# Optimization experiments

Measured on AMD Instinct MI355X. Metric: run time of the kernel, lower is better.

The kernel has to match this reference:

```python
import jax, jax.numpy as jnp
import numpy as np

B, C_IN, C_INTER, H, W_DIM = 8, 512, 256, 64, 64


def setup_inputs() -> dict:
    key = jax.random.key(0)
    k1, k2, k3, k4 = jax.random.split(key, 4)
    x = jax.random.normal(k1, (B, C_IN, H, W_DIM), dtype=jnp.float32)
    pem_feats = jax.random.normal(k2, (B, C_INTER, H * W_DIM), dtype=jnp.float32)
    # 1x1 conv weight stored as [out, in] (kernel spatial dims are 1x1)
    W = jax.random.normal(k3, (C_INTER, C_IN), dtype=jnp.float32) * (1.0 / np.sqrt(C_IN))
    bias = jax.random.normal(k4, (C_INTER,), dtype=jnp.float32) * 0.01
    return {"x": x, "pem_feats": pem_feats, "W": W, "bias": bias}


def reference(x, pem_feats, W, bias):
    b, c, h, w = x.shape
    # 1x1 conv == channel-mixing GEMM: [b, inter, h, w]
    proj = jnp.einsum('bchw,oc->bohw', x, W) + bias[None, :, None, None]
    proj = proj.reshape(b, -1, h * w)                      # [b, inter, hw]
    # weights[b,i,j] = <proj[:, i], pem[:, j]>  -> [b, hw, hw], softmax over j
    scores = jnp.einsum('bci,bcj->bij', proj, pem_feats)
    weights = jax.nn.softmax(scores, axis=-1)
    # out[b,k,i] = sum_j weights[b,j,i] * pem[b,k,j]
    eam = jnp.einsum('bji,bkj->bki', weights, pem_feats)   # [b, inter, hw]
    return eam.reshape(b, -1, h, w)
```

## Files before the change

kernel.cpp:

```cpp
#include <hip/hip_runtime.h>
#include <math.h>

#define BATCH 8
#define CIN 512
#define CO 256
#define HW 4096
#define KT 32
#define NCHUNK 128
#define NSEG 4
#define SEGC (NCHUNK / NSEG)

typedef unsigned short ushort_t;
typedef unsigned int uint_t;
typedef __bf16 v8bf __attribute__((ext_vector_type(8)));
typedef _Float16 v8h __attribute__((ext_vector_type(8)));
typedef _Float16 v4h __attribute__((ext_vector_type(4)));
typedef float v4f __attribute__((ext_vector_type(4)));
typedef ushort_t u16x8 __attribute__((ext_vector_type(8)));

__device__ __forceinline__ ushort_t f2bf(float f) {
  uint_t u = __float_as_uint(f);
  u += 0x7FFFu + ((u >> 16) & 1u);
  return (ushort_t)(u >> 16);
}
__device__ __forceinline__ float bf2f(ushort_t h) {
  return __uint_as_float(((uint_t)h) << 16);
}
__device__ __forceinline__ ushort_t f2h(float f) {
  return __builtin_bit_cast(ushort_t, (_Float16)f);
}
__device__ __forceinline__ v4f mfma16(v8bf a, v8bf b, v4f c) {
  return __builtin_amdgcn_mfma_f32_16x16x32_bf16(a, b, c, 0, 0, 0);
}
__device__ __forceinline__ v4f mfma16h(v8h a, v8h b, v4f c) {
  return __builtin_amdgcn_mfma_f32_16x16x32_f16(a, b, c, 0, 0, 0);
}
__device__ __forceinline__ v8h lds_frag_h512(const unsigned char* base, int row, int cb) {
  uint4 v = *(const uint4*)(base + row * 512 + (((cb) ^ (row & 7)) << 4));
  return __builtin_bit_cast(v8h, v);
}
__device__ __forceinline__ v8bf lds_frag128(const unsigned char* base, int row, int cb) {
  uint4 v = *(const uint4*)(base + row * 128 + (((cb) ^ (row & 7)) << 4));
  return __builtin_bit_cast(v8bf, v);
}
__device__ __forceinline__ v8h lds_frag_h16(const unsigned char* base, int row, int cb) {
  uint4 v = *(const uint4*)(base + row * 256 + (((cb) ^ (row & 15)) << 4));
  return __builtin_bit_cast(v8h, v);
}
__device__ __forceinline__ void gll16(const void* g, void* l) {
  __builtin_amdgcn_global_load_lds(
      (const __attribute__((address_space(1))) unsigned int*)g,
      (__attribute__((address_space(3))) unsigned int*)l, 16, 0, 0);
}

__global__ __launch_bounds__(256) void k_w_split(
    const float* __restrict__ W, ushort_t* __restrict__ w_hi,
    ushort_t* __restrict__ w_lo) {
  int idx = blockIdx.x * 256 + threadIdx.x;
  size_t off = (size_t)idx * 8;
  float4 v0 = *(const float4*)&W[off];
  float4 v1 = *(const float4*)&W[off + 4];
  float f[8] = {v0.x, v0.y, v0.z, v0.w, v1.x, v1.y, v1.z, v1.w};
  u16x8 h, l;
#pragma unroll
  for (int j = 0; j < 8; ++j) {
    ushort_t hh = f2bf(f[j]);
    h[j] = hh;
    l[j] = f2bf(f[j] - bf2f(hh));
  }
  *(u16x8*)&w_hi[off] = h;
  *(u16x8*)&w_lo[off] = l;
}

__global__ __launch_bounds__(256) void k_tr_x(
    const float* __restrict__ x,
    ushort_t* __restrict__ xt_hi, ushort_t* __restrict__ xt_lo) {
  __shared__ float T[64][65];
  const int i0 = blockIdx.x * 64;
  const int c0 = blockIdx.y * 64;
  const int b  = blockIdx.z;
  const int t  = threadIdx.x;
  const int cl = t >> 4;
  const int i4 = (t & 15) * 4;
#pragma unroll
  for (int r = 0; r < 4; ++r) {
    int c = c0 + r * 16 + cl;
    size_t off = ((size_t)b * CIN + c) * HW + i0 + i4;
    float4 v = *(const float4*)&x[off];
    T[r * 16 + cl][i4 + 0] = v.x;
    T[r * 16 + cl][i4 + 1] = v.y;
    T[r * 16 + cl][i4 + 2] = v.z;
    T[r * 16 + cl][i4 + 3] = v.w;
  }
  __syncthreads();
  {
    int il = t >> 2;
    int cs = (t & 3) * 16;
    u16x8 h0, h1, l0, l1;
#pragma unroll
    for (int j = 0; j < 8; ++j) {
      float f = T[cs + j][il];
      ushort_t h = f2bf(f);
      h0[j] = h;
      l0[j] = f2bf(f - bf2f(h));
    }
#pragma unroll
    for (int j = 0; j < 8; ++j) {
      float f = T[cs + 8 + j][il];
      ushort_t h = f2bf(f);
      h1[j] = h;
      l1[j] = f2bf(f - bf2f(h));
    }
    size_t ro = ((size_t)b * HW + i0 + il) * CIN + c0 + cs;
    *(u16x8*)&xt_hi[ro]     = h0;
    *(u16x8*)&xt_hi[ro + 8] = h1;
    *(u16x8*)&xt_lo[ro]     = l0;
    *(u16x8*)&xt_lo[ro + 8] = l1;
  }
}

__global__ __launch_bounds__(256, 2) void k_proj_mfma(
    const ushort_t* __restrict__ xt_hi, const ushort_t* __restrict__ xt_lo,
    const ushort_t* __restrict__ w_hi, const ushort_t* __restrict__ w_lo,
    const float* __restrict__ bias, ushort_t* __restrict__ proj_h) {
  __shared__ __align__(16) unsigned char L[4][128 * 128];
  const int bid = blockIdx.x;
  const int b = bid & 7;
  const int rest = bid >> 3;
  const int xt = rest & 31;
  const int oh = rest >> 5;
  const int x0 = xt * 128;
  const int t = threadIdx.x;
  const int lane = t & 63, wave = t >> 6;

  v4f acc[2][8];
#pragma unroll
  for (int xf = 0; xf < 2; ++xf)
#pragma unroll
    for (int of = 0; of < 8; ++of) acc[xf][of] = (v4f){0.f, 0.f, 0.f, 0.f};

  float bias_of[8];
#pragma unroll
  for (int of = 0; of < 8; ++of)
    bias_of[of] = bias[oh * 128 + of * 16 + (lane & 15)];

  for (int ch = 0; ch < 8; ++ch) {
    const int c0 = ch * 64;
#pragma unroll
    for (int i = 0; i < 4; ++i) {
      int G = i * 256 + t;
      int r = G >> 3, sl = G & 7;
      int cg = (sl ^ (r & 7)) << 3;
      size_t xsrc = ((size_t)b * HW + x0 + r) * CIN + c0 + cg;
      size_t wsrc = ((size_t)(oh * 128 + r)) * CIN + c0 + cg;
      unsigned lb = (unsigned)((i * 256 + wave * 64) << 4);
      gll16(&xt_hi[xsrc], &L[0][lb]);
      gll16(&xt_lo[xsrc], &L[1][lb]);
      gll16(&w_hi[wsrc],  &L[2][lb]);
      gll16(&w_lo[wsrc],  &L[3][lb]);
    }
    __syncthreads();
#pragma unroll
    for (int st = 0; st < 2; ++st) {
      int cb = st * 4 + (lane >> 4);
      v8bf ah0 = lds_frag128(L[0], wave * 32 + (lane & 15), cb);
      v8bf ah1 = lds_frag128(L[0], wave * 32 + 16 + (lane & 15), cb);
      v8bf al0 = lds_frag128(L[1], wave * 32 + (lane & 15), cb);
      v8bf al1 = lds_frag128(L[1], wave * 32 + 16 + (lane & 15), cb);
#pragma unroll
      for (int of = 0; of < 8; ++of) {
        v8bf bh = lds_frag128(L[2], of * 16 + (lane & 15), cb);
        v8bf bl = lds_frag128(L[3], of * 16 + (lane & 15), cb);
        acc[0][of] = mfma16(ah0, bh, acc[0][of]);
        acc[0][of] = mfma16(ah0, bl, acc[0][of]);
        acc[0][of] = mfma16(al0, bh, acc[0][of]);
        acc[1][of] = mfma16(ah1, bh, acc[1][of]);
        acc[1][of] = mfma16(ah1, bl, acc[1][of]);
        acc[1][of] = mfma16(al1, bh, acc[1][of]);
      }
    }
    __syncthreads();
  }

  ushort_t* Th = (ushort_t*)&L[0][0];
#pragma unroll
  for (int xf = 0; xf < 2; ++xf)
#pragma unroll
    for (int of = 0; of < 8; ++of)
#pragma unroll
      for (int r = 0; r < 4; ++r) {
        int x_loc = wave * 32 + xf * 16 + (lane >> 4) * 4 + r;
        int o_loc = of * 16 + (lane & 15);
        Th[x_loc * 128 + o_loc] = f2h(acc[xf][of][r] + bias_of[of]);
      }
  __syncthreads();
  {
    int row = t >> 1, half = t & 1;
    size_t off = ((size_t)b * HW + x0 + row) * CO + oh * 128 + half * 64;
#pragma unroll
    for (int j = 0; j < 8; ++j)
      *(uint4*)&proj_h[off + j * 8] =
          *(const uint4*)&Th[row * 128 + half * 64 + j * 8];
  }
}

__global__ __launch_bounds__(256) void k_tr_pem(
    const float* __restrict__ pem,
    ushort_t* __restrict__ pem_t_h, ushort_t* __restrict__ pem_h) {
  __shared__ float T[64][65];
  const int y0 = blockIdx.x * 64;
  const int c0 = blockIdx.y * 64;
  const int b  = blockIdx.z;
  const int t  = threadIdx.x;
  const int cl = t >> 4;
  const int y4 = (t & 15) * 4;
#pragma unroll
  for (int r = 0; r < 4; ++r) {
    int c = c0 + r * 16 + cl;
    size_t off = ((size_t)b * CO + c) * HW + y0 + y4;
    float4 v = *(const float4*)&pem[off];
    ushort4 h;
    h.x = f2h(v.x); h.y = f2h(v.y); h.z = f2h(v.z); h.w = f2h(v.w);
    *(ushort4*)&pem_h[off] = h;
    T[r * 16 + cl][y4 + 0] = v.x;
    T[r * 16 + cl][y4 + 1] = v.y;
    T[r * 16 + cl][y4 + 2] = v.z;
    T[r * 16 + cl][y4 + 3] = v.w;
  }
  __syncthreads();
  {
    int yl = t >> 2;
    int cs = (t & 3) * 16;
    u16x8 h0, h1;
#pragma unroll
    for (int j = 0; j < 8; ++j) h0[j] = f2h(T[cs + j][yl]);
#pragma unroll
    for (int j = 0; j < 8; ++j) h1[j] = f2h(T[cs + 8 + j][yl]);
    size_t ro = ((size_t)b * HW + y0 + yl) * CO + c0 + cs;
    *(u16x8*)&pem_t_h[ro]     = h0;
    *(u16x8*)&pem_t_h[ro + 8] = h1;
  }
}

__global__ __launch_bounds__(256, 3) void k_pass1(
    const ushort_t* __restrict__ proj_h, const ushort_t* __restrict__ pem_t_h,
    _Float16* __restrict__ Ep, float* __restrict__ m_snap,
    float* __restrict__ m_seg, float* __restrict__ d_seg,
    int nb, int b_base) {
  __shared__ __align__(16) unsigned char pbuf[2][32 * 512];
  __shared__ __align__(16) unsigned char Etr[2][32 * 256];
  const int id = blockIdx.x;
  const int brel = id % nb;
  const int b = b_base + brel;
  const int rest = id / nb;
  const int xt = rest & 31;
  const int seg = rest >> 5;
  const int x0 = xt * 128;
  const int t = threadIdx.x;
  const int lane = t & 63, wave = t >> 6;
  const int xw = x0 + wave * 32;

  v8h Ah[2][8];
#pragma unroll
  for (int xf = 0; xf < 2; ++xf) {
    const size_t ro =
        ((size_t)b * HW + xw + xf * 16 + (lane & 15)) * CO + (lane >> 4) * 8;
#pragma unroll
    for (int st = 0; st < 8; ++st)
      Ah[xf][st] = __builtin_bit_cast(v8h, *(const uint4*)&proj_h[ro + st * 32]);
  }

  float m[2][4], d[2][4];
#pragma unroll
  for (int xf = 0; xf < 2; ++xf)
#pragma unroll
    for (int r = 0; r < 4; ++r) { m[xf][r] = -3.0e38f; d[xf][r] = 0.f; }

  auto stage = [&](int bufi, int tt) {
    const int yy0 = tt * 32;
#pragma unroll
    for (int i = 0; i < 4; ++i) {
      int G = i * 256 + t;
      int r = G >> 5, sl = G & 31;
      size_t so = ((size_t)b * HW + yy0 + r) * CO + ((sl ^ (r & 7)) << 3);
      unsigned lb = (unsigned)((i * 256 + wave * 64) << 4);
      gll16(&pem_t_h[so], &pbuf[bufi][lb]);
    }
  };

  const int tt0 = seg * SEGC;
  stage(0, tt0);
  __syncthreads();

  for (int tc = 0; tc < SEGC; ++tc) {
    const int tt = tt0 + tc;
    if (tc + 1 < SEGC) stage((tc + 1) & 1, tt + 1);

    const unsigned char* bp = pbuf[tc & 1];
    v4f acc[2][2];
#pragma unroll
    for (int xf = 0; xf < 2; ++xf)
#pragma unroll
      for (int yc = 0; yc < 2; ++yc) acc[xf][yc] = (v4f){0.f, 0.f, 0.f, 0.f};

#pragma unroll
    for (int st = 0; st < 8; ++st) {
#pragma unroll
      for (int yc = 0; yc < 2; ++yc) {
        int row = yc * 16 + (lane & 15);
        int cb  = st * 4 + (lane >> 4);
        v8h bh = lds_frag_h512(bp, row, cb);
        acc[0][yc] = mfma16h(Ah[0][st], bh, acc[0][yc]);
        acc[1][yc] = mfma16h(Ah[1][st], bh, acc[1][yc]);
      }
    }

#pragma unroll
    for (int xf = 0; xf < 2; ++xf) {
      float mx8 = fmaxf(fmaxf(fmaxf(acc[xf][0][0], acc[xf][0][1]),
                              fmaxf(acc[xf][0][2], acc[xf][0][3])),
                        fmaxf(fmaxf(acc[xf][1][0], acc[xf][1][1]),
                              fmaxf(acc[xf][1][2], acc[xf][1][3])));
      float minm = fminf(fminf(m[xf][0], m[xf][1]), fminf(m[xf][2], m[xf][3]));
      if (__any(mx8 > minm + 8.0f)) {
#pragma unroll
        for (int r = 0; r < 4; ++r) {
          float rm = fmaxf(acc[xf][0][r], acc[xf][1][r]);
          rm = fmaxf(rm, __shfl_xor(rm, 1));
          rm = fmaxf(rm, __shfl_xor(rm, 2));
          rm = fmaxf(rm, __shfl_xor(rm, 4));
          rm = fmaxf(rm, __shfl_xor(rm, 8));
          float mn = fmaxf(m[xf][r], rm);
          d[xf][r] *= __expf(m[xf][r] - mn);
          m[xf][r] = mn;
        }
      }
      v4h p0, p1;
#pragma unroll
      for (int r = 0; r < 4; ++r) {
        float e0 = __expf(acc[xf][0][r] - m[xf][r]);
        float e1 = __expf(acc[xf][1][r] - m[xf][r]);
        d[xf][r] += e0 + e1;
        p0[r] = (_Float16)e0;
        p1[r] = (_Float16)e1;
      }
      {
        int gx = (wave * 32 + xf * 16 + (lane >> 4) * 4) >> 3;
        int half = (lane >> 4) & 1;
        int y0l = lane & 15, y1l = 16 + (lane & 15);
        *(uint2*)&Etr[tc & 1][y0l * 256 + ((gx ^ (y0l & 15)) << 4) + half * 8] =
            __builtin_bit_cast(uint2, p0);
        *(uint2*)&Etr[tc & 1][y1l * 256 + ((gx ^ (y1l & 15)) << 4) + half * 8] =
            __builtin_bit_cast(uint2, p1);
      }
      if ((lane & 15) == 0) {
        *(float4*)&m_snap[((size_t)b * NCHUNK + tt) * HW + xw + xf * 16 +
                          (lane >> 4) * 4] =
            make_float4(m[xf][0], m[xf][1], m[xf][2], m[xf][3]);
      }
    }
    __syncthreads();
    {
      int yr = t >> 3;
      int g0 = (t & 7) * 2, g1 = g0 + 1;
      uint4 v0 = *(uint4*)&Etr[tc & 1][yr * 256 + ((g0 ^ (yr & 15)) << 4)];
      uint4 v1 = *(uint4*)&Etr[tc & 1][yr * 256 + ((g1 ^ (yr & 15)) << 4)];
      size_t go = (((size_t)(brel * 32 + xt)) * HW + (size_t)tt * 32 + yr) * 128;
      *(uint4*)&Ep[go + g0 * 8] = v0;
      *(uint4*)&Ep[go + g1 * 8] = v1;
    }
  }

#pragma unroll
  for (int xf = 0; xf < 2; ++xf) {
    float dv[4];
#pragma unroll
    for (int r = 0; r < 4; ++r) {
      float v = d[xf][r];
      v += __shfl_xor(v, 1);
      v += __shfl_xor(v, 2);
      v += __shfl_xor(v, 4);
      v += __shfl_xor(v, 8);
      dv[r] = v;
    }
    if ((lane & 15) == 0) {
      size_t o = ((size_t)(b * NSEG + seg)) * HW + xw + xf * 16 + (lane >> 4) * 4;
      *(float4*)&m_seg[o] = make_float4(m[xf][0], m[xf][1], m[xf][2], m[xf][3]);
      *(float4*)&d_seg[o] = make_float4(dv[0], dv[1], dv[2], dv[3]);
    }
  }
}

__global__ __launch_bounds__(256) void k_red(
    const float* __restrict__ m_seg, const float* __restrict__ d_seg,
    float* __restrict__ Mx, float* __restrict__ Dinv, int b_base) {
  int idx = blockIdx.x * 256 + threadIdx.x;
  int b = b_base + (idx >> 12);
  int xx = idx & 4095;
  float ms[NSEG], ds[NSEG];
  float mm = -3.0e38f;
#pragma unroll
  for (int s = 0; s < NSEG; ++s) {
    ms[s] = m_seg[((size_t)(b * NSEG + s)) * HW + xx];
    ds[s] = d_seg[((size_t)(b * NSEG + s)) * HW + xx];
    mm = fmaxf(mm, ms[s]);
  }
  float dd = 0.f;
#pragma unroll
  for (int s = 0; s < NSEG; ++s) dd += ds[s] * __expf(ms[s] - mm);
  Mx[(size_t)b * HW + xx]   = mm;
  Dinv[(size_t)b * HW + xx] = 1.0f / dd;
}

__global__ __launch_bounds__(256, 2) void k_pass2(
    const _Float16* __restrict__ Ep, const ushort_t* __restrict__ pem_h_u,
    const float* __restrict__ m_snap, const float* __restrict__ Mx,
    const float* __restrict__ Dinv, float* __restrict__ out,
    int nb, int b_base) {
  __shared__ __align__(16) unsigned char pml[128 * 256];
  __shared__ __align__(16) unsigned char el[2][64 * 256];
  __shared__ __align__(16) _Float16 slds[2][256];
  const int id = blockIdx.x;
  const int brel = id % nb;
  const int b = b_base + brel;
  const int rest = id / nb;
  const int kh = rest & 1;
  const int yt = rest >> 1;
  const int y0 = yt * 64;
  const int t = threadIdx.x;
  const int lane = t & 63, wave = t >> 6;
  const _Float16* pem_h = (const _Float16*)pem_h_u;

  v4f oacc[2][4];
#pragma unroll
  for (int kf = 0; kf < 2; ++kf)
#pragma unroll
    for (int yf = 0; yf < 4; ++yf) oacc[kf][yf] = (v4f){0.f, 0.f, 0.f, 0.f};

  auto stage_pml = [&](int xt) {
#pragma unroll
    for (int i = 0; i < 8; ++i) {
      int G = i * 256 + t;
      int r = G >> 4, sl = G & 15;
      size_t so = ((size_t)b * CO + kh * 128 + r) * HW + xt * 128 +
                  ((sl ^ (r & 15)) << 3);
      gll16(&pem_h[so], &pml[(unsigned)((i * 256 + wave * 64) << 4)]);
    }
  };
  auto load_el = [&](int xt, uint4* ev) {
    const size_t slab = ((size_t)(brel * 32 + xt)) * HW * 128;
#pragma unroll
    for (int i = 0; i < 4; ++i) {
      int G = i * 256 + t;
      ev[i] = *(const uint4*)&Ep[slab + (size_t)(y0 + (G >> 4)) * 128 +
                                 (G & 15) * 8];
    }
  };
  auto comp_s = [&](int bufi, int xt) {
    int ttrel = t >> 7, xr = t & 127;
    int ttg = (y0 >> 5) + ttrel;
    size_t xg = (size_t)xt * 128 + xr;
    float ms = m_snap[((size_t)b * NCHUNK + ttg) * HW + xg];
    float s = __expf(ms - Mx[(size_t)b * HW + xg]) * Dinv[(size_t)b * HW + xg];
    slds[bufi][ttrel * 128 + xr] = (_Float16)s;
  };
  auto write_el = [&](int bufi, const uint4* ev) {
#pragma unroll
    for (int i = 0; i < 4; ++i) {
      int G = i * 256 + t;
      int yl = G >> 4, sl = G & 15;
      v8h e = __builtin_bit_cast(v8h, ev[i]);
      v8h s = *(const v8h*)&slds[bufi][(yl >> 5) * 128 + sl * 8];
      e = e * s;
      *(uint4*)&el[bufi][yl * 256 + ((sl ^ (yl & 15)) << 4)] =
          __builtin_bit_cast(uint4, e);
    }
  };

  uint4 ev[4];
  comp_s(0, 0);
  load_el(0, ev);
  stage_pml(0);
  __syncthreads();
  write_el(0, ev);
  comp_s(1, 1);
  __syncthreads();

  for (int xt = 0; xt < 32; ++xt) {
    const int cur = xt & 1, nxt = cur ^ 1;
    if (xt + 1 < 32) load_el(xt + 1, ev);
#pragma unroll
    for (int st = 0; st < 4; ++st) {
      int cb = st * 4 + (lane >> 4);
      v8h af0 = lds_frag_h16(pml, wave * 32 + (lane & 15), cb);
      v8h af1 = lds_frag_h16(pml, wave * 32 + 16 + (lane & 15), cb);
      v8h bf0 = lds_frag_h16(el[cur], 0 + (lane & 15), cb);
      v8h bf1 = lds_frag_h16(el[cur], 16 + (lane & 15), cb);
      v8h bf2 = lds_frag_h16(el[cur], 32 + (lane & 15), cb);
      v8h bf3 = lds_frag_h16(el[cur], 48 + (lane & 15), cb);
      oacc[0][0] = mfma16h(af0, bf0, oacc[0][0]);
      oacc[0][1] = mfma16h(af0, bf1, oacc[0][1]);
      oacc[0][2] = mfma16h(af0, bf2, oacc[0][2]);
      oacc[0][3] = mfma16h(af0, bf3, oacc[0][3]);
      oacc[1][0] = mfma16h(af1, bf0, oacc[1][0]);
      oacc[1][1] = mfma16h(af1, bf1, oacc[1][1]);
      oacc[1][2] = mfma16h(af1, bf2, oacc[1][2]);
      oacc[1][3] = mfma16h(af1, bf3, oacc[1][3]);
    }
    __syncthreads();
    if (xt + 1 < 32) {
      stage_pml(xt + 1);
      write_el(nxt, ev);
      if (xt + 2 < 32) comp_s(cur, xt + 2);
    }
    __syncthreads();
  }

#pragma unroll
  for (int kf = 0; kf < 2; ++kf)
#pragma unroll
    for (int yf = 0; yf < 4; ++yf)
#pragma unroll
      for (int r = 0; r < 4; ++r) {
        int k = kh * 128 + wave * 32 + kf * 16 + (lane >> 4) * 4 + r;
        int y = y0 + yf * 16 + (lane & 15);
        out[((size_t)b * CO + k) * HW + y] = oacc[kf][yf][r];
      }
}

__global__ __launch_bounds__(256) void k_proj(
    const float* __restrict__ x, const float* __restrict__ W,
    const float* __restrict__ bias, float* __restrict__ proj) {
  __shared__ float As[KT][68];
  __shared__ float Bs[KT][68];
  const int i0 = blockIdx.x * 64;
  const int o0 = blockIdx.y * 64;
  const int b  = blockIdx.z;
  const int t  = threadIdx.x;
  const int tx = t & 15, ty = t >> 4;
  const float* xb = x + (size_t)b * CIN * HW;
  float acc[4][4] = {};
  for (int c0 = 0; c0 < CIN; c0 += KT) {
#pragma unroll
    for (int l = 0; l < 8; ++l) {
      int idx = t + l * 256;
      int o = idx >> 5;
      int c = idx & 31;
      As[c][o] = W[(size_t)(o0 + o) * CIN + c0 + c];
    }
#pragma unroll
    for (int l = 0; l < 2; ++l) {
      int idx4 = t + l * 256;
      int c = idx4 >> 4;
      int i4 = idx4 & 15;
      *(float4*)&Bs[c][i4 * 4] =
          *(const float4*)&xb[(size_t)(c0 + c) * HW + i0 + i4 * 4];
    }
    __syncthreads();
#pragma unroll
    for (int c = 0; c < KT; ++c) {
      float4 a  = *(const float4*)&As[c][tx * 4];
      float4 bv = *(const float4*)&Bs[c][ty * 4];
      float av[4] = {a.x, a.y, a.z, a.w};
      float bb[4] = {bv.x, bv.y, bv.z, bv.w};
#pragma unroll
      for (int u = 0; u < 4; ++u)
#pragma unroll
        for (int v = 0; v < 4; ++v) acc[u][v] += av[u] * bb[v];
    }
    __syncthreads();
  }
  float* pbout = proj + (size_t)b * CO * HW;
#pragma unroll
  for (int u = 0; u < 4; ++u) {
    int o = o0 + tx * 4 + u;
    float bsv = bias[o];
    float4 r;
    r.x = acc[u][0] + bsv; r.y = acc[u][1] + bsv;
    r.z = acc[u][2] + bsv; r.w = acc[u][3] + bsv;
    *(float4*)&pbout[(size_t)o * HW + i0 + ty * 4] = r;
  }
}

__global__ __launch_bounds__(256) void k_stats(
    const float* __restrict__ proj, const float* __restrict__ pem,
    float* __restrict__ Mx, float* __restrict__ Dinv) {
  __shared__ float As[KT][68];
  __shared__ float Bs[KT][68];
  __shared__ float MsS[64][17];
  __shared__ float DsS[64][17];
  const int x0 = blockIdx.x * 64;
  const int b  = blockIdx.y;
  const int t  = threadIdx.x;
  const int tx = t & 15, ty = t >> 4;
  const float* pj = proj + (size_t)b * CO * HW;
  const float* pe = pem + (size_t)b * CO * HW;
  float m[4], d[4];
#pragma unroll
  for (int u = 0; u < 4; ++u) { m[u] = -3.0e38f; d[u] = 0.f; }
  for (int y0 = 0; y0 < HW; y0 += 64) {
    float s[4][4] = {};
    for (int c0 = 0; c0 < CO; c0 += KT) {
#pragma unroll
      for (int l = 0; l < 2; ++l) {
        int idx4 = t + l * 256;
        int c = idx4 >> 4, w4 = idx4 & 15;
        *(float4*)&As[c][w4 * 4] =
            *(const float4*)&pj[(size_t)(c0 + c) * HW + x0 + w4 * 4];
        *(float4*)&Bs[c][w4 * 4] =
            *(const float4*)&pe[(size_t)(c0 + c) * HW + y0 + w4 * 4];
      }
      __syncthreads();
#pragma unroll
      for (int c = 0; c < KT; ++c) {
        float4 a  = *(const float4*)&As[c][tx * 4];
        float4 bv = *(const float4*)&Bs[c][ty * 4];
        float av[4] = {a.x, a.y, a.z, a.w};
        float bb[4] = {bv.x, bv.y, bv.z, bv.w};
#pragma unroll
        for (int u = 0; u < 4; ++u)
#pragma unroll
          for (int v = 0; v < 4; ++v) s[u][v] += av[u] * bb[v];
      }
      __syncthreads();
    }
#pragma unroll
    for (int u = 0; u < 4; ++u) {
      float mv = fmaxf(fmaxf(s[u][0], s[u][1]), fmaxf(s[u][2], s[u][3]));
      if (mv > m[u]) { d[u] *= __expf(m[u] - mv); m[u] = mv; }
      d[u] += __expf(s[u][0] - m[u]) + __expf(s[u][1] - m[u]) +
              __expf(s[u][2] - m[u]) + __expf(s[u][3] - m[u]);
    }
  }
#pragma unroll
  for (int u = 0; u < 4; ++u) { MsS[tx * 4 + u][ty] = m[u]; DsS[tx * 4 + u][ty] = d[u]; }
  __syncthreads();
  if (t < 64) {
    float mm = -3.0e38f;
#pragma unroll
    for (int i = 0; i < 16; ++i) mm = fmaxf(mm, MsS[t][i]);
    float dd = 0.f;
#pragma unroll
    for (int i = 0; i < 16; ++i) dd += DsS[t][i] * __expf(MsS[t][i] - mm);
    Mx[(size_t)b * HW + x0 + t]   = mm;
    Dinv[(size_t)b * HW + x0 + t] = 1.0f / dd;
  }
}

__global__ __launch_bounds__(256) void k_out(
    const float* __restrict__ proj, const float* __restrict__ pem,
    const float* __restrict__ Mx, const float* __restrict__ Dinv,
    float* __restrict__ out) {
  __shared__ float As[KT][68];
  __shared__ float Bs[KT][68];
  __shared__ float E[64][68];
  const int y0 = blockIdx.x * 64;
  const int b  = blockIdx.y;
  const int t  = threadIdx.x;
  const int tx = t & 15, ty = t >> 4;
  const int kg = t >> 3, yg = t & 7;
  const float* pj = proj + (size_t)b * CO * HW;
  const float* pe = pem + (size_t)b * CO * HW;
  const float* Mb = Mx + (size_t)b * HW;
  const float* Db = Dinv + (size_t)b * HW;
  float acc[8][8] = {};
  for (int x0 = 0; x0 < HW; x0 += 64) {
    float s[4][4] = {};
    for (int c0 = 0; c0 < CO; c0 += KT) {
#pragma unroll
      for (int l = 0; l < 2; ++l) {
        int idx4 = t + l * 256;
        int c = idx4 >> 4, w4 = idx4 & 15;
        *(float4*)&As[c][w4 * 4] =
            *(const float4*)&pj[(size_t)(c0 + c) * HW + x0 + w4 * 4];
        *(float4*)&Bs[c][w4 * 4] =
            *(const float4*)&pe[(size_t)(c0 + c) * HW + y0 + w4 * 4];
      }
      __syncthreads();
#pragma unroll
      for (int c = 0; c < KT; ++c) {
        float4 a  = *(const float4*)&As[c][tx * 4];
        float4 bv = *(const float4*)&Bs[c][ty * 4];
        float av[4] = {a.x, a.y, a.z, a.w};
        float bb[4] = {bv.x, bv.y, bv.z, bv.w};
#pragma unroll
        for (int u = 0; u < 4; ++u)
#pragma unroll
          for (int v = 0; v < 4; ++v) s[u][v] += av[u] * bb[v];
      }
      __syncthreads();
    }
#pragma unroll
    for (int u = 0; u < 4; ++u) {
      int xr = x0 + tx * 4 + u;
      float mm = Mb[xr];
      float di = Db[xr];
      E[tx * 4 + u][ty * 4 + 0] = __expf(s[u][0] - mm) * di;
      E[tx * 4 + u][ty * 4 + 1] = __expf(s[u][1] - mm) * di;
      E[tx * 4 + u][ty * 4 + 2] = __expf(s[u][2] - mm) * di;
      E[tx * 4 + u][ty * 4 + 3] = __expf(s[u][3] - mm) * di;
    }
    __syncthreads();
    for (int xi = 0; xi < 64; xi += 4) {
      float4 p[8];
#pragma unroll
      for (int u = 0; u < 8; ++u)
        p[u] = *(const float4*)&pe[(size_t)(kg * 8 + u) * HW + x0 + xi];
#pragma unroll
      for (int j = 0; j < 4; ++j) {
        float4 e0 = *(const float4*)&E[xi + j][yg * 8];
        float4 e1 = *(const float4*)&E[xi + j][yg * 8 + 4];
        float evv[8] = {e0.x, e0.y, e0.z, e0.w, e1.x, e1.y, e1.z, e1.w};
#pragma unroll
        for (int u = 0; u < 8; ++u) {
          float a = (j == 0) ? p[u].x : (j == 1) ? p[u].y : (j == 2) ? p[u].z : p[u].w;
#pragma unroll
          for (int v = 0; v < 8; ++v) acc[u][v] += a * evv[v];
        }
      }
    }
    __syncthreads();
  }
#pragma unroll
  for (int u = 0; u < 8; ++u) {
    int k = kg * 8 + u;
    float4 r0, r1;
    r0.x = acc[u][0]; r0.y = acc[u][1]; r0.z = acc[u][2]; r0.w = acc[u][3];
    r1.x = acc[u][4]; r1.y = acc[u][5]; r1.z = acc[u][6]; r1.w = acc[u][7];
    float* ob = out + ((size_t)b * CO + k) * HW + y0 + yg * 8;
    *(float4*)&ob[0] = r0;
    *(float4*)&ob[4] = r1;
  }
}

extern "C" void kernel_launch(void* const* d_in, const int* in_sizes, int n_in,
                              void* d_out, int out_size, void* d_ws, size_t ws_size,
                              hipStream_t stream) {
  const float* x    = (const float*)d_in[0];
  const float* pem  = (const float*)d_in[1];
  const float* W    = (const float*)d_in[2];
  const float* bias = (const float*)d_in[3];
  float* out = (float*)d_out;

  const size_t NS   = (size_t)BATCH * HW * CO;
  const size_t NS2  = (size_t)BATCH * HW * CIN;
  const size_t HWB  = (size_t)BATCH * HW;
  const size_t SNAP = (size_t)BATCH * NCHUNK * HW;
  const size_t SEGN = (size_t)BATCH * NSEG * HW;

  unsigned char* basep = (unsigned char*)d_ws;
  ushort_t* proj_h   = (ushort_t*)basep;
  ushort_t* pem_t_h  = proj_h + NS;
  ushort_t* pem_h    = pem_t_h + NS;
  float*    Mx       = (float*)(pem_h + NS);
  float*    Dinv     = Mx + HWB;
  float*    m_seg    = Dinv + HWB;
  float*    d_seg    = m_seg + SEGN;
  float*    m_snap   = d_seg + SEGN;
  _Float16* Ep       = (_Float16*)(m_snap + SNAP);

  ushort_t* xt_hi = (ushort_t*)Ep;
  ushort_t* xt_lo = xt_hi + NS2;
  ushort_t* w_hi  = xt_lo + NS2;
  ushort_t* w_lo  = w_hi + (size_t)CO * CIN;

  const size_t base_need = 3 * NS * 2 + 2 * HWB * 4 + 2 * SEGN * 4 + SNAP * 4;
  const size_t e_full    = (size_t)BATCH * HW * HW * 2;

  int rounds, nb;
  if (ws_size >= base_need + e_full)          { rounds = 1; nb = 8; }
  else if (ws_size >= base_need + e_full / 2) { rounds = 2; nb = 4; }
  else {
    float* proj = (float*)d_ws;
    float* Mx2  = proj + NS;
    float* Di2  = Mx2 + HWB;
    const size_t need = (NS + 2 * HWB) * sizeof(float);
    if (ws_size < need) return;
    k_proj <<<dim3(HW / 64, CO / 64, BATCH), 256, 0, stream>>>(x, W, bias, proj);
    k_stats<<<dim3(HW / 64, BATCH),          256, 0, stream>>>(proj, pem, Mx2, Di2);
    k_out  <<<dim3(HW / 64, BATCH),          256, 0, stream>>>(proj, pem, Mx2, Di2, out);
    return;
  }

  k_w_split<<<64, 256, 0, stream>>>(W, w_hi, w_lo);
  k_tr_x<<<dim3(HW / 64, CIN / 64, BATCH), 256, 0, stream>>>(x, xt_hi, xt_lo);
  k_proj_mfma<<<512, 256, 0, stream>>>(xt_hi, xt_lo, w_hi, w_lo, bias, proj_h);
  k_tr_pem<<<dim3(HW / 64, CO / 64, BATCH), 256, 0, stream>>>(
      pem, pem_t_h, pem_h);

  for (int rd = 0; rd < rounds; ++rd) {
    int b_base = rd * nb;
    k_pass1<<<nb * 128, 256, 0, stream>>>(proj_h, pem_t_h,
                                          Ep, m_snap, m_seg, d_seg, nb, b_base);
    k_red<<<nb * 16, 256, 0, stream>>>(m_seg, d_seg, Mx, Dinv, b_base);
    k_pass2<<<nb * 128, 256, 0, stream>>>(Ep, pem_h, m_snap,
                                          Mx, Dinv, out, nb, b_base);
  }
}
```

Measured before the change: 360.7 us.

## Replace materialized exp matrix with stats pass plus fused recompute kernel

Drops the pass that wrote the full fp16 exp-score matrix and per-chunk max snapshots to global memory. A stats-only kernel now computes the column max and denominator, which are folded into a single log-sum-exp per column. A fused kernel then recomputes the scores per 64x64 tile, applies the exp-normalize and multiplies by pem on the fly. This removes a very large global write and read in exchange for computing the QK GEMM twice, and the stats kernel's tile is widened to 256 columns per block.

```diff
diff --git a/kernel.cpp b/kernel.cpp
--- a/kernel.cpp
+++ b/kernel.cpp
@@ -6,9 +6,8 @@
 #define CO 256
 #define HW 4096
 #define KT 32
-#define NCHUNK 128
 #define NSEG 4
-#define SEGC (NCHUNK / NSEG)
+#define SEGC 32
 
 typedef unsigned short ushort_t;
 typedef unsigned int uint_t;
@@ -39,13 +38,13 @@
   uint4 v = *(const uint4*)(base + row * 512 + (((cb) ^ (row & 7)) << 4));
   return __builtin_bit_cast(v8h, v);
 }
+__device__ __forceinline__ v8h lds_frag_h128(const unsigned char* base, int row, int cb) {
+  uint4 v = *(const uint4*)(base + row * 128 + (((cb) ^ (row & 7)) << 4));
+  return __builtin_bit_cast(v8h, v);
+}
 __device__ __forceinline__ v8bf lds_frag128(const unsigned char* base, int row, int cb) {
   uint4 v = *(const uint4*)(base + row * 128 + (((cb) ^ (row & 7)) << 4));
   return __builtin_bit_cast(v8bf, v);
-}
-__device__ __forceinline__ v8h lds_frag_h16(const unsigned char* base, int row, int cb) {
-  uint4 v = *(const uint4*)(base + row * 256 + (((cb) ^ (row & 15)) << 4));
-  return __builtin_bit_cast(v8h, v);
 }
 __device__ __forceinline__ void gll16(const void* g, void* l) {
   __builtin_amdgcn_global_load_lds(
@@ -242,27 +241,23 @@
   }
 }
 
-__global__ __launch_bounds__(256, 3) void k_pass1(
+__global__ __launch_bounds__(256, 2) void k_stats_f16(
     const ushort_t* __restrict__ proj_h, const ushort_t* __restrict__ pem_t_h,
-    _Float16* __restrict__ Ep, float* __restrict__ m_snap,
-    float* __restrict__ m_seg, float* __restrict__ d_seg,
-    int nb, int b_base) {
+    float* __restrict__ m_seg, float* __restrict__ d_seg) {
   __shared__ __align__(16) unsigned char pbuf[2][32 * 512];
-  __shared__ __align__(16) unsigned char Etr[2][32 * 256];
   const int id = blockIdx.x;
-  const int brel = id % nb;
-  const int b = b_base + brel;
-  const int rest = id / nb;
-  const int xt = rest & 31;
-  const int seg = rest >> 5;
-  const int x0 = xt * 128;
+  const int b = id & 7;
+  const int rest = id >> 3;
+  const int xt = rest & 15;
+  const int seg = rest >> 4;
+  const int x0 = xt * 256;
   const int t = threadIdx.x;
   const int lane = t & 63, wave = t >> 6;
-  const int xw = x0 + wave * 32;
-
-  v8h Ah[2][8];
-#pragma unroll
-  for (int xf = 0; xf < 2; ++xf) {
+  const int xw = x0 + wave * 64;
+
+  v8h Ah[4][8];
+#pragma unroll
+  for (int xf = 0; xf < 4; ++xf) {
     const size_t ro =
         ((size_t)b * HW + xw + xf * 16 + (lane & 15)) * CO + (lane >> 4) * 8;
 #pragma unroll
@@ -270,9 +265,9 @@
       Ah[xf][st] = __builtin_bit_cast(v8h, *(const uint4*)&proj_h[ro + st * 32]);
   }
 
-  float m[2][4], d[2][4];
-#pragma unroll
-  for (int xf = 0; xf < 2; ++xf)
+  float m[4][4], d[4][4];
+#pragma unroll
+  for (int xf = 0; xf < 4; ++xf)
 #pragma unroll
     for (int r = 0; r < 4; ++r) { m[xf][r] = -3.0e38f; d[xf][r] = 0.f; }
 
@@ -293,13 +288,12 @@
   __syncthreads();
 
   for (int tc = 0; tc < SEGC; ++tc) {
-    const int tt = tt0 + tc;
-    if (tc + 1 < SEGC) stage((tc + 1) & 1, tt + 1);
+    if (tc + 1 < SEGC) stage((tc + 1) & 1, tt0 + tc + 1);
 
     const unsigned char* bp = pbuf[tc & 1];
-    v4f acc[2][2];
-#pragma unroll
-    for (int xf = 0; xf < 2; ++xf)
+    v4f acc[4][2];
+#pragma unroll
+    for (int xf = 0; xf < 4; ++xf)
 #pragma unroll
       for (int yc = 0; yc < 2; ++yc) acc[xf][yc] = (v4f){0.f, 0.f, 0.f, 0.f};
 
@@ -307,16 +301,16 @@
     for (int st = 0; st < 8; ++st) {
 #pragma unroll
       for (int yc = 0; yc < 2; ++yc) {
-        int row = yc * 16 + (lane & 15);
-        int cb  = st * 4 + (lane >> 4);
-        v8h bh = lds_frag_h512(bp, row, cb);
+        v8h bh = lds_frag_h512(bp, yc * 16 + (lane & 15), st * 4 + (lane >> 4));
         acc[0][yc] = mfma16h(Ah[0][st], bh, acc[0][yc]);
         acc[1][yc] = mfma16h(Ah[1][st], bh, acc[1][yc]);
-      }
-    }
-
-#pragma unroll
-    for (int xf = 0; xf < 2; ++xf) {
+        acc[2][yc] = mfma16h(Ah[2][st], bh, acc[2][yc]);
+        acc[3][yc] = mfma16h(Ah[3][st], bh, acc[3][yc]);
+      }
+    }
+
+#pragma unroll
+    for (int xf = 0; xf < 4; ++xf) {
       float mx8 = fmaxf(fmaxf(fmaxf(acc[xf][0][0], acc[xf][0][1]),
                               fmaxf(acc[xf][0][2], acc[xf][0][3])),
                         fmaxf(fmaxf(acc[xf][1][0], acc[xf][1][1]),
@@ -335,44 +329,16 @@
           m[xf][r] = mn;
         }
       }
-      v4h p0, p1;
-#pragma unroll
-      for (int r = 0; r < 4; ++r) {
-        float e0 = __expf(acc[xf][0][r] - m[xf][r]);
-        float e1 = __expf(acc[xf][1][r] - m[xf][r]);
-        d[xf][r] += e0 + e1;
-        p0[r] = (_Float16)e0;
-        p1[r] = (_Float16)e1;
-      }
-      {
-        int gx = (wave * 32 + xf * 16 + (lane >> 4) * 4) >> 3;
-        int half = (lane >> 4) & 1;
-        int y0l = lane & 15, y1l = 16 + (lane & 15);
-        *(uint2*)&Etr[tc & 1][y0l * 256 + ((gx ^ (y0l & 15)) << 4) + half * 8] =
-            __builtin_bit_cast(uint2, p0);
-        *(uint2*)&Etr[tc & 1][y1l * 256 + ((gx ^ (y1l & 15)) << 4) + half * 8] =
-            __builtin_bit_cast(uint2, p1);
-      }
-      if ((lane & 15) == 0) {
-        *(float4*)&m_snap[((size_t)b * NCHUNK + tt) * HW + xw + xf * 16 +
-                          (lane >> 4) * 4] =
-            make_float4(m[xf][0], m[xf][1], m[xf][2], m[xf][3]);
-      }
-    }
-    __syncthreads();
-    {
-      int yr = t >> 3;
-      int g0 = (t & 7) * 2, g1 = g0 + 1;
-      uint4 v0 = *(uint4*)&Etr[tc & 1][yr * 256 + ((g0 ^ (yr & 15)) << 4)];
-      uint4 v1 = *(uint4*)&Etr[tc & 1][yr * 256 + ((g1 ^ (yr & 15)) << 4)];
-      size_t go = (((size_t)(brel * 32 + xt)) * HW + (size_t)tt * 32 + yr) * 128;
-      *(uint4*)&Ep[go + g0 * 8] = v0;
-      *(uint4*)&Ep[go + g1 * 8] = v1;
-    }
-  }
-
-#pragma unroll
-  for (int xf = 0; xf < 2; ++xf) {
+#pragma unroll
+      for (int r = 0; r < 4; ++r)
+        d[xf][r] += __expf(acc[xf][0][r] - m[xf][r]) +
+                    __expf(acc[xf][1][r] - m[xf][r]);
+    }
+    __syncthreads();
+  }
+
+#pragma unroll
+  for (int xf = 0; xf < 4; ++xf) {
     float dv[4];
 #pragma unroll
     for (int r = 0; r < 4; ++r) {
@@ -391,11 +357,11 @@
   }
 }
 
-__global__ __launch_bounds__(256) void k_red(
+__global__ __launch_bounds__(256) void k_red2(
     const float* __restrict__ m_seg, const float* __restrict__ d_seg,
-    float* __restrict__ Mx, float* __restrict__ Dinv, int b_base) {
+    float* __restrict__ Cx) {
   int idx = blockIdx.x * 256 + threadIdx.x;
-  int b = b_base + (idx >> 12);
+  int b = idx >> 12;
   int xx = idx & 4095;
   float ms[NSEG], ds[NSEG];
   float mm = -3.0e38f;
@@ -408,123 +374,117 @@
   float dd = 0.f;
 #pragma unroll
   for (int s = 0; s < NSEG; ++s) dd += ds[s] * __expf(ms[s] - mm);
-  Mx[(size_t)b * HW + xx]   = mm;
-  Dinv[(size_t)b * HW + xx] = 1.0f / dd;
-}
-
-__global__ __launch_bounds__(256, 2) void k_pass2(
-    const _Float16* __restrict__ Ep, const ushort_t* __restrict__ pem_h_u,
-    const float* __restrict__ m_snap, const float* __restrict__ Mx,
-    const float* __restrict__ Dinv, float* __restrict__ out,
-    int nb, int b_base) {
-  __shared__ __align__(16) unsigned char pml[128 * 256];
-  __shared__ __align__(16) unsigned char el[2][64 * 256];
-  __shared__ __align__(16) _Float16 slds[2][256];
+  Cx[(size_t)b * HW + xx] = mm + __logf(dd);
+}
+
+__global__ __launch_bounds__(256, 2) void k_fused(
+    const ushort_t* __restrict__ proj_h, const ushort_t* __restrict__ pem_t_h,
+    const ushort_t* __restrict__ pem_h, const float* __restrict__ Cx,
+    float* __restrict__ out) {
+  __shared__ __align__(16) unsigned char Lp[64 * 512];
+  __shared__ __align__(16) unsigned char Lk[256 * 128];
+  __shared__ __align__(16) unsigned char Le[64 * 128];
+  __shared__ float Clds[64];
   const int id = blockIdx.x;
-  const int brel = id % nb;
-  const int b = b_base + brel;
-  const int rest = id / nb;
-  const int kh = rest & 1;
-  const int yt = rest >> 1;
+  const int b = id & 7;
+  const int yt = id >> 3;
   const int y0 = yt * 64;
   const int t = threadIdx.x;
   const int lane = t & 63, wave = t >> 6;
-  const _Float16* pem_h = (const _Float16*)pem_h_u;
-
-  v4f oacc[2][4];
-#pragma unroll
-  for (int kf = 0; kf < 2; ++kf)
-#pragma unroll
-    for (int yf = 0; yf < 4; ++yf) oacc[kf][yf] = (v4f){0.f, 0.f, 0.f, 0.f};
-
-  auto stage_pml = [&](int xt) {
+
+  v8h Bres[8];
+  {
+    const size_t ro =
+        ((size_t)b * HW + y0 + wave * 16 + (lane & 15)) * CO + (lane >> 4) * 8;
+#pragma unroll
+    for (int st = 0; st < 8; ++st)
+      Bres[st] = __builtin_bit_cast(v8h, *(const uint4*)&pem_t_h[ro + st * 32]);
+  }
+
+  v4f pv[4][4];
+#pragma unroll
+  for (int kf = 0; kf < 4; ++kf)
+#pragma unroll
+    for (int yf = 0; yf < 4; ++yf) pv[kf][yf] = (v4f){0.f, 0.f, 0.f, 0.f};
+
+  for (int xt = 0; xt < 64; ++xt) {
+    const int x0 = xt * 64;
+    __syncthreads();
 #pragma unroll
     for (int i = 0; i < 8; ++i) {
       int G = i * 256 + t;
-      int r = G >> 4, sl = G & 15;
-      size_t so = ((size_t)b * CO + kh * 128 + r) * HW + xt * 128 +
-                  ((sl ^ (r & 15)) << 3);
-      gll16(&pem_h[so], &pml[(unsigned)((i * 256 + wave * 64) << 4)]);
-    }
-  };
-  auto load_el = [&](int xt, uint4* ev) {
-    const size_t slab = ((size_t)(brel * 32 + xt)) * HW * 128;
-#pragma unroll
-    for (int i = 0; i < 4; ++i) {
+      int r = G >> 5, sl = G & 31;
+      size_t so = ((size_t)b * HW + x0 + r) * CO + ((sl ^ (r & 7)) << 3);
+      gll16(&proj_h[so], &Lp[(unsigned)((i * 256 + wave * 64) << 4)]);
+    }
+#pragma unroll
+    for (int i = 0; i < 8; ++i) {
       int G = i * 256 + t;
-      ev[i] = *(const uint4*)&Ep[slab + (size_t)(y0 + (G >> 4)) * 128 +
-                                 (G & 15) * 8];
-    }
-  };
-  auto comp_s = [&](int bufi, int xt) {
-    int ttrel = t >> 7, xr = t & 127;
-    int ttg = (y0 >> 5) + ttrel;
-    size_t xg = (size_t)xt * 128 + xr;
-    float ms = m_snap[((size_t)b * NCHUNK + ttg) * HW + xg];
-    float s = __expf(ms - Mx[(size_t)b * HW + xg]) * Dinv[(size_t)b * HW + xg];
-    slds[bufi][ttrel * 128 + xr] = (_Float16)s;
-  };
-  auto write_el = [&](int bufi, const uint4* ev) {
-#pragma unroll
-    for (int i = 0; i < 4; ++i) {
-      int G = i * 256 + t;
-      int yl = G >> 4, sl = G & 15;
-      v8h e = __builtin_bit_cast(v8h, ev[i]);
-      v8h s = *(const v8h*)&slds[bufi][(yl >> 5) * 128 + sl * 8];
-      e = e * s;
-      *(uint4*)&el[bufi][yl * 256 + ((sl ^ (yl & 15)) << 4)] =
-          __builtin_bit_cast(uint4, e);
-    }
-  };
-
-  uint4 ev[4];
-  comp_s(0, 0);
-  load_el(0, ev);
-  stage_pml(0);
-  __syncthreads();
-  write_el(0, ev);
-  comp_s(1, 1);
-  __syncthreads();
-
-  for (int xt = 0; xt < 32; ++xt) {
-    const int cur = xt & 1, nxt = cur ^ 1;
-    if (xt + 1 < 32) load_el(xt + 1, ev);
-#pragma unroll
-    for (int st = 0; st < 4; ++st) {
+      int r = G >> 3, sl = G & 7;
+      size_t so = ((size_t)b * CO + r) * HW + x0 + ((sl ^ (r & 7)) << 3);
+      gll16(&pem_h[so], &Lk[(unsigned)((i * 256 + wave * 64) << 4)]);
+    }
+    if (t < 64) Clds[t] = Cx[(size_t)b * HW + x0 + t];
+    __syncthreads();
+
+    v4f s[4];
+#pragma unroll
+    for (int xf = 0; xf < 4; ++xf) s[xf] = (v4f){0.f, 0.f, 0.f, 0.f};
+#pragma unroll
+    for (int st = 0; st < 8; ++st) {
       int cb = st * 4 + (lane >> 4);
-      v8h af0 = lds_frag_h16(pml, wave * 32 + (lane & 15), cb);
-      v8h af1 = lds_frag_h16(pml, wave * 32 + 16 + (lane & 15), cb);
-      v8h bf0 = lds_frag_h16(el[cur], 0 + (lane & 15), cb);
-      v8h bf1 = lds_frag_h16(el[cur], 16 + (lane & 15), cb);
-      v8h bf2 = lds_frag_h16(el[cur], 32 + (lane & 15), cb);
-      v8h bf3 = lds_frag_h16(el[cur], 48 + (lane & 15), cb);
-      oacc[0][0] = mfma16h(af0, bf0, oacc[0][0]);
-      oacc[0][1] = mfma16h(af0, bf1, oacc[0][1]);
-      oacc[0][2] = mfma16h(af0, bf2, oacc[0][2]);
-      oacc[0][3] = mfma16h(af0, bf3, oacc[0][3]);
-      oacc[1][0] = mfma16h(af1, bf0, oacc[1][0]);
-      oacc[1][1] = mfma16h(af1, bf1, oacc[1][1]);
-      oacc[1][2] = mfma16h(af1, bf2, oacc[1][2]);
-      oacc[1][3] = mfma16h(af1, bf3, oacc[1][3]);
-    }
-    __syncthreads();
-    if (xt + 1 < 32) {
-      stage_pml(xt + 1);
-      write_el(nxt, ev);
-      if (xt + 2 < 32) comp_s(cur, xt + 2);
-    }
-    __syncthreads();
-  }
-
-#pragma unroll
-  for (int kf = 0; kf < 2; ++kf)
+      v8h bh = Bres[st];
+      s[0] = mfma16h(lds_frag_h512(Lp, 0  + (lane & 15), cb), bh, s[0]);
+      s[1] = mfma16h(lds_frag_h512(Lp, 16 + (lane & 15), cb), bh, s[1]);
+      s[2] = mfma16h(lds_frag_h512(Lp, 32 + (lane & 15), cb), bh, s[2]);
+      s[3] = mfma16h(lds_frag_h512(Lp, 48 + (lane & 15), cb), bh, s[3]);
+    }
+    {
+      int yl = wave * 16 + (lane & 15);
+      int half = (lane >> 4) & 1;
+      int gbase = (lane >> 4) >> 1;
+#pragma unroll
+      for (int xf = 0; xf < 4; ++xf) {
+        float4 c4 = *(const float4*)&Clds[xf * 16 + (lane >> 4) * 4];
+        float cc[4] = {c4.x, c4.y, c4.z, c4.w};
+        v4h p;
+#pragma unroll
+        for (int r = 0; r < 4; ++r) p[r] = (_Float16)__expf(s[xf][r] - cc[r]);
+        int gx = xf * 2 + gbase;
+        *(uint2*)(Le + yl * 128 + ((gx ^ (yl & 7)) << 4) + half * 8) =
+            __builtin_bit_cast(uint2, p);
+      }
+    }
+    __syncthreads();
+
+    const int kb = wave * 64;
+#pragma unroll
+    for (int ks = 0; ks < 2; ++ks) {
+      int cb = ks * 4 + (lane >> 4);
+      v8h e0 = lds_frag_h128(Le, 0  + (lane & 15), cb);
+      v8h e1 = lds_frag_h128(Le, 16 + (lane & 15), cb);
+      v8h e2 = lds_frag_h128(Le, 32 + (lane & 15), cb);
+      v8h e3 = lds_frag_h128(Le, 48 + (lane & 15), cb);
+#pragma unroll
+      for (int kf = 0; kf < 4; ++kf) {
+        v8h af = lds_frag_h128(Lk, kb + kf * 16 + (lane & 15), cb);
+        pv[kf][0] = mfma16h(af, e0, pv[kf][0]);
+        pv[kf][1] = mfma16h(af, e1, pv[kf][1]);
+        pv[kf][2] = mfma16h(af, e2, pv[kf][2]);
+        pv[kf][3] = mfma16h(af, e3, pv[kf][3]);
+      }
+    }
+  }
+
+#pragma unroll
+  for (int kf = 0; kf < 4; ++kf)
 #pragma unroll
     for (int yf = 0; yf < 4; ++yf)
 #pragma unroll
       for (int r = 0; r < 4; ++r) {
-        int k = kh * 128 + wave * 32 + kf * 16 + (lane >> 4) * 4 + r;
+        int k = wave * 64 + kf * 16 + (lane >> 4) * 4 + r;
         int y = y0 + yf * 16 + (lane & 15);
-        out[((size_t)b * CO + k) * HW + y] = oacc[kf][yf][r];
+        out[((size_t)b * CO + k) * HW + y] = pv[kf][yf][r];
       }
 }
 
@@ -745,37 +705,29 @@
   const size_t NS   = (size_t)BATCH * HW * CO;
   const size_t NS2  = (size_t)BATCH * HW * CIN;
   const size_t HWB  = (size_t)BATCH * HW;
-  const size_t SNAP = (size_t)BATCH * NCHUNK * HW;
   const size_t SEGN = (size_t)BATCH * NSEG * HW;
+  const size_t WN   = (size_t)CO * CIN;
 
   unsigned char* basep = (unsigned char*)d_ws;
   ushort_t* proj_h   = (ushort_t*)basep;
   ushort_t* pem_t_h  = proj_h + NS;
   ushort_t* pem_h    = pem_t_h + NS;
-  float*    Mx       = (float*)(pem_h + NS);
-  float*    Dinv     = Mx + HWB;
-  float*    m_seg    = Dinv + HWB;
+  float*    Cxp      = (float*)(pem_h + NS);
+  float*    m_seg    = Cxp + HWB;
   float*    d_seg    = m_seg + SEGN;
-  float*    m_snap   = d_seg + SEGN;
-  _Float16* Ep       = (_Float16*)(m_snap + SNAP);
-
-  ushort_t* xt_hi = (ushort_t*)Ep;
-  ushort_t* xt_lo = xt_hi + NS2;
-  ushort_t* w_hi  = xt_lo + NS2;
-  ushort_t* w_lo  = w_hi + (size_t)CO * CIN;
-
-  const size_t base_need = 3 * NS * 2 + 2 * HWB * 4 + 2 * SEGN * 4 + SNAP * 4;
-  const size_t e_full    = (size_t)BATCH * HW * HW * 2;
-
-  int rounds, nb;
-  if (ws_size >= base_need + e_full)          { rounds = 1; nb = 8; }
-  else if (ws_size >= base_need + e_full / 2) { rounds = 2; nb = 4; }
-  else {
+  ushort_t* xt_hi    = (ushort_t*)(d_seg + SEGN);
+  ushort_t* xt_lo    = xt_hi + NS2;
+  ushort_t* w_hi     = xt_lo + NS2;
+  ushort_t* w_lo     = w_hi + WN;
+
+  const size_t need = 3 * NS * 2 + HWB * 4 + 2 * SEGN * 4 + 2 * NS2 * 2 + 2 * WN * 2;
+
+  if (ws_size < need) {
     float* proj = (float*)d_ws;
     float* Mx2  = proj + NS;
     float* Di2  = Mx2 + HWB;
-    const size_t need = (NS + 2 * HWB) * sizeof(float);
-    if (ws_size < need) return;
+    const size_t need_f = (NS + 2 * HWB) * sizeof(float);
+    if (ws_size < need_f) return;
     k_proj <<<dim3(HW / 64, CO / 64, BATCH), 256, 0, stream>>>(x, W, bias, proj);
     k_stats<<<dim3(HW / 64, BATCH),          256, 0, stream>>>(proj, pem, Mx2, Di2);
     k_out  <<<dim3(HW / 64, BATCH),          256, 0, stream>>>(proj, pem, Mx2, Di2, out);
@@ -785,15 +737,9 @@
   k_w_split<<<64, 256, 0, stream>>>(W, w_hi, w_lo);
   k_tr_x<<<dim3(HW / 64, CIN / 64, BATCH), 256, 0, stream>>>(x, xt_hi, xt_lo);
   k_proj_mfma<<<512, 256, 0, stream>>>(xt_hi, xt_lo, w_hi, w_lo, bias, proj_h);
-  k_tr_pem<<<dim3(HW / 64, CO / 64, BATCH), 256, 0, stream>>>(
-      pem, pem_t_h, pem_h);
-
-  for (int rd = 0; rd < rounds; ++rd) {
-    int b_base = rd * nb;
-    k_pass1<<<nb * 128, 256, 0, stream>>>(proj_h, pem_t_h,
-                                          Ep, m_snap, m_seg, d_seg, nb, b_base);
-    k_red<<<nb * 16, 256, 0, stream>>>(m_seg, d_seg, Mx, Dinv, b_base);
-    k_pass2<<<nb * 128, 256, 0, stream>>>(Ep, pem_h, m_snap,
-                                          Mx, Dinv, out, nb, b_base);
-  }
-}
+  k_tr_pem<<<dim3(HW / 64, CO / 64, BATCH), 256, 0, stream>>>(pem, pem_t_h, pem_h);
+
+  k_stats_f16<<<512, 256, 0, stream>>>(proj_h, pem_t_h, m_seg, d_seg);
+  k_red2<<<128, 256, 0, stream>>>(m_seg, d_seg, Cxp);
+  k_fused<<<512, 256, 0, stream>>>(proj_h, pem_t_h, pem_h, Cxp, out);
+}
```

Result: slower. 369.8 us (+2.5%).
